# Kernel optimization log

Measured on AMD Instinct MI355X. Metric: run time of the kernel, lower is better.

Reference implementation:

```python
import jax, jax.numpy as jnp
import numpy as np
from jax import lax

B, T, H, F, K, NB, MAXLEN = 32, 1024, 384, 384, 3, 256, 2048


def _ln(x, g, b, eps=1e-5):
    m = jnp.mean(x, axis=-1, keepdims=True)
    v = jnp.var(x, axis=-1, keepdims=True)
    return (x - m) * lax.rsqrt(v + eps) * g + b


def _conv(x, w, b):
    # x: (B, T, Cin), w: (K, Cin, Cout); SAME padding == torch padding=(K-1)//2 for K=3, stride 1
    y = lax.conv_general_dilated(x, w, (1,), 'SAME', dimension_numbers=('NWC', 'WIO', 'NWC'))
    return y + b


def _predictor(x, mask, w1, b1, g1, be1, w2, b2, g2, be2, wo, bo):
    h = _ln(jax.nn.relu(_conv(x, w1, b1)), g1, be1)
    h = _ln(jax.nn.relu(_conv(h, w2, b2)), g2, be2)
    out = jnp.einsum('btf,f->bt', h, wo) + bo  # Linear(F -> 1).squeeze(-1)
    return jnp.where(mask, 0.0, out)


def _length_regulate(x, dur, max_len):
    # vectorized equivalent of torch per-sample expand+cat+pad
    csum = jnp.cumsum(dur, axis=1)                      # (B, T)
    total = csum[:, -1]                                 # (B,) = mel_len
    frames = jnp.arange(max_len)                        # (M,)
    # frame f belongs to phoneme i with csum[i-1] <= f < csum[i]
    idx = jax.vmap(lambda c: jnp.searchsorted(c, frames, side='right'))(csum)  # (B, M)
    idx = jnp.clip(idx, 0, x.shape[1] - 1)
    out = jnp.take_along_axis(x, idx[:, :, None], axis=1)                      # (B, M, H)
    valid = (frames[None, :] < total[:, None]).astype(x.dtype)                 # zero-pad tail
    return out * valid[:, :, None], total


def setup_inputs() -> dict:
    key = jax.random.key(0)
    ks = iter(jax.random.split(key, 64))
    nk = lambda: next(ks)
    d = {}
    d['x'] = jax.random.normal(nk(), (B, T, H), jnp.float32)
    d['src_mask'] = jnp.zeros((B, T), jnp.bool_)
    d['duration'] = jax.random.randint(nk(), (B, T), 0, 4)
    d['max_len'] = MAXLEN
    for p in ('dp', 'pp', 'ep'):
        d[p + '_w1'] = jax.random.normal(nk(), (K, H, F), jnp.float32) * 0.02
        d[p + '_b1'] = jnp.zeros((F,), jnp.float32)
        d[p + '_g1'] = jnp.ones((F,), jnp.float32)
        d[p + '_be1'] = jnp.zeros((F,), jnp.float32)
        d[p + '_w2'] = jax.random.normal(nk(), (K, F, F), jnp.float32) * 0.02
        d[p + '_b2'] = jnp.zeros((F,), jnp.float32)
        d[p + '_g2'] = jnp.ones((F,), jnp.float32)
        d[p + '_be2'] = jnp.zeros((F,), jnp.float32)
        d[p + '_wo'] = jax.random.normal(nk(), (F,), jnp.float32) * 0.02
        d[p + '_bo'] = jnp.zeros((1,), jnp.float32)
    d['pitch_bins'] = jnp.linspace(0.0, 1.0, NB - 1, dtype=jnp.float32)
    d['energy_bins'] = jnp.linspace(0.0, 1.0, NB - 1, dtype=jnp.float32)
    d['pitch_emb'] = jax.random.normal(nk(), (NB, H), jnp.float32) * 0.02
    d['energy_emb'] = jax.random.normal(nk(), (NB, H), jnp.float32) * 0.02
    d['pitch_target'] = jax.random.uniform(nk(), (B, T), jnp.float32)
    d['energy_target'] = jax.random.uniform(nk(), (B, T), jnp.float32)
    return d


def reference(x, src_mask, duration, max_len,
              dp_w1, dp_b1, dp_g1, dp_be1, dp_w2, dp_b2, dp_g2, dp_be2, dp_wo, dp_bo,
              pp_w1, pp_b1, pp_g1, pp_be1, pp_w2, pp_b2, pp_g2, pp_be2, pp_wo, pp_bo,
              ep_w1, ep_b1, ep_g1, ep_be1, ep_w2, ep_b2, ep_g2, ep_be2, ep_wo, ep_bo,
              pitch_bins, energy_bins, pitch_emb, energy_emb, pitch_target, energy_target):
    log_dur = _predictor(x, src_mask, dp_w1, dp_b1, dp_g1, dp_be1, dp_w2, dp_b2, dp_g2, dp_be2, dp_wo, dp_bo)
    # phoneme-level pitch (target path: bucketize target, torch.bucketize right=False == searchsorted left)
    pitch_pred = _predictor(x, src_mask, pp_w1, pp_b1, pp_g1, pp_be1, pp_w2, pp_b2, pp_g2, pp_be2, pp_wo, pp_bo)
    x = x + pitch_emb[jnp.searchsorted(pitch_bins, pitch_target, side='left')]
    # phoneme-level energy (predictor sees x AFTER pitch embedding add, as in torch)
    energy_pred = _predictor(x, src_mask, ep_w1, ep_b1, ep_g1, ep_be1, ep_w2, ep_b2, ep_g2, ep_be2, ep_wo, ep_bo)
    x = x + energy_emb[jnp.searchsorted(energy_bins, energy_target, side='left')]
    x_out, mel_len = _length_regulate(x, duration, max_len)
    return (x_out, pitch_pred, energy_pred, log_dur, mel_len)
```

## Files before the change

kernel.cpp:

```cpp
#include <hip/hip_runtime.h>

#define B_ 32
#define T_ 1024
#define C_ 384
#define MAXLEN_ 2048
#define NBINS_ 255
#define WPK1 442368
#define BTC  (32 * 1024 * 384)
#define ARS 392

typedef __attribute__((ext_vector_type(8))) short short8v;
typedef __attribute__((ext_vector_type(4))) float floatx4;

__device__ __forceinline__ unsigned short f2bf(float f) {
    unsigned u = __float_as_uint(f);
    u += 0x7fffu + ((u >> 16) & 1u);
    return (unsigned short)(u >> 16);
}

struct CvP {
    const float* xf;
    const unsigned short* xb;
    const unsigned short* wpk;
    const float* bias[3];
    const float* gamma[3];
    const float* beta[3];
    const float* wo[3];
    const float* bo[3];
    unsigned short* hout;
    float* pred[3];
    const float* pbins;
    const float* pemb;
    const float* ptgt;
    int final_flag;
};

__global__ __launch_bounds__(256, 2) void conv_mfma3(CvP P)
{
    __shared__ unsigned short As[66 * ARS];
    float* rsum = (float*)As;
    float* rsq  = rsum + 256;

    const int tid  = threadIdx.x;
    const int wave = tid >> 6;
    const int lane = tid & 63;
    const int lq   = lane >> 4;
    const int ln   = lane & 15;
    const int p    = blockIdx.x >> 9;
    const int bi   = blockIdx.x & 511;
    const int b    = bi >> 4;
    const int t0   = (bi & 15) << 6;
    const int nb   = wave * 96;

    const unsigned short* bbase =
        P.wpk + (size_t)p * WPK1 + wave * 3072 + (size_t)lane * 8;
    short8v bA[6], bB[6];
#pragma unroll
    for (int nt = 0; nt < 6; ++nt) {
        bA[nt] = *(const short8v*)(bbase + (nt << 9));
        bB[nt] = *(const short8v*)(bbase + 12288 + (nt << 9));
    }

    if (!P.final_flag) {
        const bool fuse_emb = (p == 2);
        for (int i = tid; i < 66 * 48; i += 256) {
            const int row = i / 48;
            const int c   = i - row * 48;
            const int t   = t0 - 1 + row;
            short8v v = (short8v){0,0,0,0,0,0,0,0};
            if ((unsigned)t < (unsigned)T_) {
                const float* sp = P.xf + ((size_t)(b << 10) + t) * C_ + c * 8;
                float f[8];
                *(float4*)&f[0] = *(const float4*)sp;
                *(float4*)&f[4] = *(const float4*)(sp + 4);
                if (fuse_emb) {
                    const float tg = P.ptgt[(b << 10) + t];
                    int lo = 0, hi = NBINS_;
                    while (lo < hi) {
                        const int mid = (lo + hi) >> 1;
                        if (P.pbins[mid] < tg) lo = mid + 1; else hi = mid;
                    }
                    const float* er = P.pemb + (size_t)lo * C_ + c * 8;
#pragma unroll
                    for (int j = 0; j < 8; ++j) f[j] += er[j];
                }
#pragma unroll
                for (int j = 0; j < 8; ++j) v[j] = (short)f2bf(f[j]);
            }
            *(short8v*)&As[row * ARS + c * 8] = v;
        }
    } else {
        const unsigned short* xb = P.xb + (size_t)p * BTC;
        for (int i = tid; i < 66 * 48; i += 256) {
            const int row = i / 48;
            const int c   = i - row * 48;
            const int t   = t0 - 1 + row;
            short8v v = (short8v){0,0,0,0,0,0,0,0};
            if ((unsigned)t < (unsigned)T_)
                v = *(const short8v*)(xb + ((size_t)(b << 10) + t) * C_ + c * 8);
            *(short8v*)&As[row * ARS + c * 8] = v;
        }
    }
    __syncthreads();

    floatx4 acc[24];
#pragma unroll
    for (int i = 0; i < 24; ++i) acc[i] = (floatx4){0.f, 0.f, 0.f, 0.f};

    const unsigned short* abase = &As[ln * ARS + lq * 8];
    const unsigned short* bpA = bbase + 2 * 12288;
    const unsigned short* bpB = bbase + 3 * 12288;

#pragma unroll
    for (int kc = 0; kc < 3; ++kc) {
#pragma unroll
        for (int h2 = 0; h2 < 6; ++h2) {
            const int hb = h2 * 64;
            const int r  = kc * 12 + h2 * 2;
            {
                short8v afrag[4];
#pragma unroll
                for (int mt = 0; mt < 4; ++mt)
                    afrag[mt] = *(const short8v*)(abase + (mt * 16 + kc) * ARS + hb);
#pragma unroll
                for (int mt = 0; mt < 4; ++mt)
#pragma unroll
                    for (int nt = 0; nt < 6; ++nt)
                        acc[mt * 6 + nt] = __builtin_amdgcn_mfma_f32_16x16x32_bf16(
                            afrag[mt], bA[nt], acc[mt * 6 + nt], 0, 0, 0);
                if (r + 2 < 36) {
#pragma unroll
                    for (int nt = 0; nt < 6; ++nt)
                        bA[nt] = *(const short8v*)(bpA + (nt << 9));
                    bpA += 24576;
                }
            }
            {
                short8v afrag[4];
#pragma unroll
                for (int mt = 0; mt < 4; ++mt)
                    afrag[mt] = *(const short8v*)(abase + (mt * 16 + kc) * ARS + hb + 32);
#pragma unroll
                for (int mt = 0; mt < 4; ++mt)
#pragma unroll
                    for (int nt = 0; nt < 6; ++nt)
                        acc[mt * 6 + nt] = __builtin_amdgcn_mfma_f32_16x16x32_bf16(
                            afrag[mt], bB[nt], acc[mt * 6 + nt], 0, 0, 0);
                if (r + 3 < 36) {
#pragma unroll
                    for (int nt = 0; nt < 6; ++nt)
                        bB[nt] = *(const short8v*)(bpB + (nt << 9));
                    bpB += 24576;
                }
            }
        }
    }
    __syncthreads();

    float bcol[6], gcol[6], becol[6], wcol[6];
#pragma unroll
    for (int nt = 0; nt < 6; ++nt) {
        const int col = nb + nt * 16 + ln;
        bcol[nt]  = P.bias[p][col];
        gcol[nt]  = P.gamma[p][col];
        becol[nt] = P.beta[p][col];
        wcol[nt]  = P.final_flag ? P.wo[p][col] : 0.f;
    }

#pragma unroll
    for (int mt = 0; mt < 4; ++mt) {
#pragma unroll
        for (int rg = 0; rg < 4; ++rg) {
            float s = 0.f, q = 0.f;
#pragma unroll
            for (int nt = 0; nt < 6; ++nt) {
                float v = acc[mt * 6 + nt][rg] + bcol[nt];
                v = v > 0.f ? v : 0.f;
                acc[mt * 6 + nt][rg] = v;
                s += v; q += v * v;
            }
#pragma unroll
            for (int off = 1; off < 16; off <<= 1) {
                s += __shfl_xor(s, off, 64);
                q += __shfl_xor(q, off, 64);
            }
            if (ln == mt * 4 + rg) {
                rsum[wave * 64 + mt * 16 + lq * 4 + rg] = s;
                rsq [wave * 64 + mt * 16 + lq * 4 + rg] = q;
            }
        }
    }
    __syncthreads();

    float mean_[16], rstd_[16];
#pragma unroll
    for (int mt = 0; mt < 4; ++mt) {
#pragma unroll
        for (int rg = 0; rg < 4; ++rg) {
            const int row = mt * 16 + lq * 4 + rg;
            const float s = rsum[row] + rsum[64 + row] + rsum[128 + row] + rsum[192 + row];
            const float q = rsq[row] + rsq[64 + row] + rsq[128 + row] + rsq[192 + row];
            const float m = s * (1.f / 384.f);
            const float var = q * (1.f / 384.f) - m * m;
            mean_[mt * 4 + rg] = m;
            rstd_[mt * 4 + rg] = rsqrtf(var + 1e-5f);
        }
    }

    if (!P.final_flag) {
        unsigned short* hout = P.hout + (size_t)p * BTC;
#pragma unroll
        for (int mt = 0; mt < 4; ++mt)
#pragma unroll
            for (int rg = 0; rg < 4; ++rg) {
                const float m = mean_[mt * 4 + rg], rs = rstd_[mt * 4 + rg];
                const int grow = (bi << 6) + mt * 16 + lq * 4 + rg;
#pragma unroll
                for (int nt = 0; nt < 6; ++nt) {
                    const float v = (acc[mt * 6 + nt][rg] - m) * rs * gcol[nt] + becol[nt];
                    hout[(size_t)grow * C_ + nb + nt * 16 + ln] = f2bf(v);
                }
            }
    } else {
        __syncthreads();
#pragma unroll
        for (int mt = 0; mt < 4; ++mt) {
#pragma unroll
            for (int rg = 0; rg < 4; ++rg) {
                const float m = mean_[mt * 4 + rg], rs = rstd_[mt * 4 + rg];
                float pr = 0.f;
#pragma unroll
                for (int nt = 0; nt < 6; ++nt)
                    pr += ((acc[mt * 6 + nt][rg] - m) * rs * gcol[nt] + becol[nt]) * wcol[nt];
#pragma unroll
                for (int off = 1; off < 16; off <<= 1)
                    pr += __shfl_xor(pr, off, 64);
                if (ln == mt * 4 + rg)
                    rsum[wave * 64 + mt * 16 + lq * 4 + rg] = pr;
            }
        }
        __syncthreads();
        if (tid < 64)
            P.pred[p][(bi << 6) + tid] =
                rsum[tid] + rsum[64 + tid] + rsum[128 + tid] + rsum[192 + tid] + P.bo[p][0];
    }
}

#define WSS 388
__global__ __launch_bounds__(256) void pack_w_kernel(
    const float* __restrict__ s0, const float* __restrict__ s1,
    const float* __restrict__ s2, const float* __restrict__ s3,
    const float* __restrict__ s4, const float* __restrict__ s5,
    unsigned short* __restrict__ dst)
{
    __shared__ float ws[32 * WSS];
    const int blk  = blockIdx.x;
    const int wsel = blk / 36;
    const int r    = blk - wsel * 36;
    const float* src = wsel == 0 ? s0 : wsel == 1 ? s1 : wsel == 2 ? s2
                     : wsel == 3 ? s3 : wsel == 4 ? s4 : s5;
    const int tid = threadIdx.x;

    const float* sb = src + (size_t)r * 32 * C_;
    for (int i4 = tid; i4 < 3072; i4 += 256) {
        const int k  = i4 / 96;
        const int n4 = i4 - k * 96;
        *(float4*)&ws[k * WSS + n4 * 4] = *(const float4*)(sb + (size_t)k * C_ + n4 * 4);
    }
    __syncthreads();

    unsigned short* db = dst + (size_t)wsel * WPK1 + (size_t)r * 12288;
    for (int c = tid; c < 1536; c += 256) {
        const int lane = c & 63;
        const int wnt  = c >> 6;
        const int ln   = lane & 15;
        const int lq   = lane >> 4;
        const int n    = (wnt / 6) * 96 + (wnt % 6) * 16 + ln;
        ushort4 o0, o1;
        unsigned short e[8];
#pragma unroll
        for (int j = 0; j < 8; ++j)
            e[j] = f2bf(ws[(lq * 8 + j) * WSS + n]);
        o0 = make_ushort4(e[0], e[1], e[2], e[3]);
        o1 = make_ushort4(e[4], e[5], e[6], e[7]);
        *(ushort4*)(db + wnt * 512 + lane * 8)     = o0;
        *(ushort4*)(db + wnt * 512 + lane * 8 + 4) = o1;
    }
}

__global__ __launch_bounds__(256) void cumsum_idx_kernel(
    const int* __restrict__ dur,
    const float* __restrict__ pbins, const float* __restrict__ ptgt,
    const float* __restrict__ ebins, const float* __restrict__ etgt,
    int* __restrict__ xidx, float* __restrict__ mel_len)
{
    __shared__ int cs[T_];
    __shared__ int part[256];
    __shared__ float pb[NBINS_], eb[NBINS_];
    const int b = blockIdx.x;
    const int tid = threadIdx.x;
    if (tid < NBINS_) { pb[tid] = pbins[tid]; eb[tid] = ebins[tid]; }
    int l[4];
    int s = 0;
#pragma unroll
    for (int i = 0; i < 4; ++i) { l[i] = dur[(b << 10) + tid * 4 + i]; s += l[i]; }
    part[tid] = s;
    __syncthreads();
    for (int off = 1; off < 256; off <<= 1) {
        int u = 0;
        if (tid >= off) u = part[tid - off];
        __syncthreads();
        part[tid] += u;
        __syncthreads();
    }
    const int incl = part[tid];
    int run = incl - s;
#pragma unroll
    for (int i = 0; i < 4; ++i) {
        run += l[i];
        cs[tid * 4 + i] = run;
    }
    if (tid == 255) mel_len[b] = (float)incl;
    __syncthreads();
    const int total = cs[T_ - 1];
    for (int f = tid; f < MAXLEN_; f += 256) {
        int pk = -1;
        if (f < total) {
            int lo = 0, hi = T_;
            while (lo < hi) {
                const int mid = (lo + hi) >> 1;
                if (cs[mid] <= f) lo = mid + 1; else hi = mid;
            }
            const int t = lo > T_ - 1 ? T_ - 1 : lo;
            const int row = (b << 10) + t;
            const float ptg = ptgt[row];
            int plo = 0, phi = NBINS_;
            while (plo < phi) {
                const int mid = (plo + phi) >> 1;
                if (pb[mid] < ptg) plo = mid + 1; else phi = mid;
            }
            const float etg = etgt[row];
            int elo = 0, ehi = NBINS_;
            while (elo < ehi) {
                const int mid = (elo + ehi) >> 1;
                if (eb[mid] < etg) elo = mid + 1; else ehi = mid;
            }
            pk = t | (plo << 10) | (elo << 19);
        }
        xidx[(b << 11) + f] = pk;
    }
}

__global__ __launch_bounds__(256) void length_reg_kernel(
    const float* __restrict__ x, const int* __restrict__ xidx,
    const float* __restrict__ pemb, const float* __restrict__ eemb,
    float* __restrict__ out)
{
    const int g    = blockIdx.x * 256 + threadIdx.x;
    const int c4   = g % 96;
    const int rest = g / 96;
    const int frame = rest & (MAXLEN_ - 1);
    const int b     = rest >> 11;
    const int pk = xidx[(b << 11) + frame];
    float4 v = make_float4(0.f, 0.f, 0.f, 0.f);
    if (pk >= 0) {
        const int t   = pk & 1023;
        const int plo = (pk >> 10) & 511;
        const int elo = (pk >> 19) & 511;
        v = *(const float4*)(x + ((size_t)(b << 10) + t) * C_ + c4 * 4);
        const float4 pe = *(const float4*)(pemb + (size_t)plo * C_ + c4 * 4);
        const float4 ee = *(const float4*)(eemb + (size_t)elo * C_ + c4 * 4);
        v.x += pe.x + ee.x; v.y += pe.y + ee.y;
        v.z += pe.z + ee.z; v.w += pe.w + ee.w;
    }
    *(float4*)(out + (size_t)g * 4) = v;
}

extern "C" void kernel_launch(void* const* d_in, const int* in_sizes, int n_in,
                              void* d_out, int out_size, void* d_ws, size_t ws_size,
                              hipStream_t stream)
{
    const float* x        = (const float*)d_in[0];
    const int*   duration = (const int*)d_in[2];
    const float* P[3][10];
    for (int p = 0; p < 3; ++p)
        for (int q = 0; q < 10; ++q)
            P[p][q] = (const float*)d_in[4 + p * 10 + q];
    const float* pitch_bins    = (const float*)d_in[34];
    const float* energy_bins   = (const float*)d_in[35];
    const float* pitch_emb     = (const float*)d_in[36];
    const float* energy_emb    = (const float*)d_in[37];
    const float* pitch_target  = (const float*)d_in[38];
    const float* energy_target = (const float*)d_in[39];

    float* out_x      = (float*)d_out;
    float* out_pitch  = out_x + (size_t)B_ * MAXLEN_ * C_;
    float* out_energy = out_pitch + B_ * T_;
    float* out_logdur = out_energy + B_ * T_;
    float* out_mellen = out_logdur + B_ * T_;

    unsigned short* h1b = (unsigned short*)out_x;

    unsigned short* wpk = (unsigned short*)d_ws;
    int* xidx = (int*)(wpk + (size_t)6 * WPK1);

    const dim3 blk(256);

    pack_w_kernel<<<216, blk, 0, stream>>>(
        P[0][0], P[0][4], P[1][0], P[1][4], P[2][0], P[2][4], wpk);

    CvP P1;
    P1.xf = x; P1.xb = nullptr; P1.wpk = wpk;
    for (int p = 0; p < 3; ++p) {
        P1.bias[p]  = P[p][1];
        P1.gamma[p] = P[p][2];
        P1.beta[p]  = P[p][3];
        P1.wo[p]    = nullptr;
        P1.bo[p]    = nullptr;
        P1.pred[p]  = nullptr;
    }
    P1.hout = h1b;
    P1.pbins = pitch_bins; P1.pemb = pitch_emb; P1.ptgt = pitch_target;
    P1.final_flag = 0;

    CvP P2;
    P2.xf = nullptr; P2.xb = h1b; P2.wpk = wpk + (size_t)3 * WPK1;
    for (int p = 0; p < 3; ++p) {
        P2.bias[p]  = P[p][5];
        P2.gamma[p] = P[p][6];
        P2.beta[p]  = P[p][7];
        P2.wo[p]    = P[p][8];
        P2.bo[p]    = P[p][9];
    }
    P2.pred[0] = out_logdur; P2.pred[1] = out_pitch; P2.pred[2] = out_energy;
    P2.hout = nullptr;
    P2.pbins = nullptr; P2.pemb = nullptr; P2.ptgt = nullptr;
    P2.final_flag = 1;

    conv_mfma3<<<1536, blk, 0, stream>>>(P1);
    conv_mfma3<<<1536, blk, 0, stream>>>(P2);

    cumsum_idx_kernel<<<B_, blk, 0, stream>>>(
        duration, pitch_bins, pitch_target, energy_bins, energy_target,
        xidx, out_mellen);
    length_reg_kernel<<<24576, blk, 0, stream>>>(
        x, xidx, pitch_emb, energy_emb, out_x);
}
```

Before: 467.6 us.

## Split conv N-dimension across six waves and hoist pitch bucketize per row

```diff
diff --git a/kernel.cpp b/kernel.cpp
--- a/kernel.cpp
+++ b/kernel.cpp
@@ -35,11 +35,12 @@
     int final_flag;
 };
 
-__global__ __launch_bounds__(256, 2) void conv_mfma3(CvP P)
+__global__ __launch_bounds__(384, 3) void conv_mfma3(CvP P)
 {
     __shared__ unsigned short As[66 * ARS];
+    __shared__ int embi[66];
     float* rsum = (float*)As;
-    float* rsq  = rsum + 256;
+    float* rsq  = rsum + 384;
 
     const int tid  = threadIdx.x;
     const int wave = tid >> 6;
@@ -50,48 +51,60 @@
     const int bi   = blockIdx.x & 511;
     const int b    = bi >> 4;
     const int t0   = (bi & 15) << 6;
-    const int nb   = wave * 96;
+    const int nb   = wave << 6;
 
     const unsigned short* bbase =
-        P.wpk + (size_t)p * WPK1 + wave * 3072 + (size_t)lane * 8;
-    short8v bA[6], bB[6];
-#pragma unroll
-    for (int nt = 0; nt < 6; ++nt) {
+        P.wpk + (size_t)p * WPK1 + (size_t)(wave << 11) + (size_t)lane * 8;
+    short8v bA[4], bB[4];
+#pragma unroll
+    for (int nt = 0; nt < 4; ++nt) {
         bA[nt] = *(const short8v*)(bbase + (nt << 9));
         bB[nt] = *(const short8v*)(bbase + 12288 + (nt << 9));
     }
 
     if (!P.final_flag) {
         const bool fuse_emb = (p == 2);
-        for (int i = tid; i < 66 * 48; i += 256) {
+        if (fuse_emb) {
+            if (tid < 66) {
+                const int t = t0 - 1 + tid;
+                int lo = 0;
+                if ((unsigned)t < (unsigned)T_) {
+                    const float tg = P.ptgt[(b << 10) + t];
+                    int hi = NBINS_;
+                    while (lo < hi) {
+                        const int mid = (lo + hi) >> 1;
+                        if (P.pbins[mid] < tg) lo = mid + 1; else hi = mid;
+                    }
+                }
+                embi[tid] = lo;
+            }
+            __syncthreads();
+        }
+        for (int i = tid; i < 66 * 48; i += 384) {
             const int row = i / 48;
             const int c   = i - row * 48;
             const int t   = t0 - 1 + row;
-            short8v v = (short8v){0,0,0,0,0,0,0,0};
+            uint4 pv = make_uint4(0u, 0u, 0u, 0u);
             if ((unsigned)t < (unsigned)T_) {
                 const float* sp = P.xf + ((size_t)(b << 10) + t) * C_ + c * 8;
                 float f[8];
                 *(float4*)&f[0] = *(const float4*)sp;
                 *(float4*)&f[4] = *(const float4*)(sp + 4);
                 if (fuse_emb) {
-                    const float tg = P.ptgt[(b << 10) + t];
-                    int lo = 0, hi = NBINS_;
-                    while (lo < hi) {
-                        const int mid = (lo + hi) >> 1;
-                        if (P.pbins[mid] < tg) lo = mid + 1; else hi = mid;
-                    }
-                    const float* er = P.pemb + (size_t)lo * C_ + c * 8;
+                    const float* er = P.pemb + (size_t)embi[row] * C_ + c * 8;
 #pragma unroll
                     for (int j = 0; j < 8; ++j) f[j] += er[j];
                 }
-#pragma unroll
-                for (int j = 0; j < 8; ++j) v[j] = (short)f2bf(f[j]);
-            }
-            *(short8v*)&As[row * ARS + c * 8] = v;
+                asm("v_cvt_pk_bf16_f32 %0, %1, %2" : "=v"(pv.x) : "v"(f[0]), "v"(f[1]));
+                asm("v_cvt_pk_bf16_f32 %0, %1, %2" : "=v"(pv.y) : "v"(f[2]), "v"(f[3]));
+                asm("v_cvt_pk_bf16_f32 %0, %1, %2" : "=v"(pv.z) : "v"(f[4]), "v"(f[5]));
+                asm("v_cvt_pk_bf16_f32 %0, %1, %2" : "=v"(pv.w) : "v"(f[6]), "v"(f[7]));
+            }
+            *(uint4*)&As[row * ARS + c * 8] = pv;
         }
     } else {
         const unsigned short* xb = P.xb + (size_t)p * BTC;
-        for (int i = tid; i < 66 * 48; i += 256) {
+        for (int i = tid; i < 66 * 48; i += 384) {
             const int row = i / 48;
             const int c   = i - row * 48;
             const int t   = t0 - 1 + row;
@@ -103,9 +116,9 @@
     }
     __syncthreads();
 
-    floatx4 acc[24];
-#pragma unroll
-    for (int i = 0; i < 24; ++i) acc[i] = (floatx4){0.f, 0.f, 0.f, 0.f};
+    floatx4 acc[16];
+#pragma unroll
+    for (int i = 0; i < 16; ++i) acc[i] = (floatx4){0.f, 0.f, 0.f, 0.f};
 
     const unsigned short* abase = &As[ln * ARS + lq * 8];
     const unsigned short* bpA = bbase + 2 * 12288;
@@ -125,12 +138,12 @@
 #pragma unroll
                 for (int mt = 0; mt < 4; ++mt)
 #pragma unroll
-                    for (int nt = 0; nt < 6; ++nt)
-                        acc[mt * 6 + nt] = __builtin_amdgcn_mfma_f32_16x16x32_bf16(
-                            afrag[mt], bA[nt], acc[mt * 6 + nt], 0, 0, 0);
+                    for (int nt = 0; nt < 4; ++nt)
+                        acc[mt * 4 + nt] = __builtin_amdgcn_mfma_f32_16x16x32_bf16(
+                            afrag[mt], bA[nt], acc[mt * 4 + nt], 0, 0, 0);
                 if (r + 2 < 36) {
 #pragma unroll
-                    for (int nt = 0; nt < 6; ++nt)
+                    for (int nt = 0; nt < 4; ++nt)
                         bA[nt] = *(const short8v*)(bpA + (nt << 9));
                     bpA += 24576;
                 }
@@ -143,12 +156,12 @@
 #pragma unroll
                 for (int mt = 0; mt < 4; ++mt)
 #pragma unroll
-                    for (int nt = 0; nt < 6; ++nt)
-                        acc[mt * 6 + nt] = __builtin_amdgcn_mfma_f32_16x16x32_bf16(
-                            afrag[mt], bB[nt], acc[mt * 6 + nt], 0, 0, 0);
+                    for (int nt = 0; nt < 4; ++nt)
+                        acc[mt * 4 + nt] = __builtin_amdgcn_mfma_f32_16x16x32_bf16(
+                            afrag[mt], bB[nt], acc[mt * 4 + nt], 0, 0, 0);
                 if (r + 3 < 36) {
 #pragma unroll
-                    for (int nt = 0; nt < 6; ++nt)
+                    for (int nt = 0; nt < 4; ++nt)
                         bB[nt] = *(const short8v*)(bpB + (nt << 9));
                     bpB += 24576;
                 }
@@ -157,9 +170,9 @@
     }
     __syncthreads();
 
-    float bcol[6], gcol[6], becol[6], wcol[6];
-#pragma unroll
-    for (int nt = 0; nt < 6; ++nt) {
+    float bcol[4], gcol[4], becol[4], wcol[4];
+#pragma unroll
+    for (int nt = 0; nt < 4; ++nt) {
         const int col = nb + nt * 16 + ln;
         bcol[nt]  = P.bias[p][col];
         gcol[nt]  = P.gamma[p][col];
@@ -173,10 +186,10 @@
         for (int rg = 0; rg < 4; ++rg) {
             float s = 0.f, q = 0.f;
 #pragma unroll
-            for (int nt = 0; nt < 6; ++nt) {
-                float v = acc[mt * 6 + nt][rg] + bcol[nt];
+            for (int nt = 0; nt < 4; ++nt) {
+                float v = acc[mt * 4 + nt][rg] + bcol[nt];
                 v = v > 0.f ? v : 0.f;
-                acc[mt * 6 + nt][rg] = v;
+                acc[mt * 4 + nt][rg] = v;
                 s += v; q += v * v;
             }
 #pragma unroll
@@ -198,8 +211,12 @@
 #pragma unroll
         for (int rg = 0; rg < 4; ++rg) {
             const int row = mt * 16 + lq * 4 + rg;
-            const float s = rsum[row] + rsum[64 + row] + rsum[128 + row] + rsum[192 + row];
-            const float q = rsq[row] + rsq[64 + row] + rsq[128 + row] + rsq[192 + row];
+            float s = 0.f, q = 0.f;
+#pragma unroll
+            for (int w = 0; w < 6; ++w) {
+                s += rsum[w * 64 + row];
+                q += rsq [w * 64 + row];
+            }
             const float m = s * (1.f / 384.f);
             const float var = q * (1.f / 384.f) - m * m;
             mean_[mt * 4 + rg] = m;
@@ -215,10 +232,15 @@
             for (int rg = 0; rg < 4; ++rg) {
                 const float m = mean_[mt * 4 + rg], rs = rstd_[mt * 4 + rg];
                 const int grow = (bi << 6) + mt * 16 + lq * 4 + rg;
-#pragma unroll
-                for (int nt = 0; nt < 6; ++nt) {
-                    const float v = (acc[mt * 6 + nt][rg] - m) * rs * gcol[nt] + becol[nt];
-                    hout[(size_t)grow * C_ + nb + nt * 16 + ln] = f2bf(v);
+                unsigned short* hb_ = hout + (size_t)grow * C_ + nb + ln;
+#pragma unroll
+                for (int n2 = 0; n2 < 2; ++n2) {
+                    const float v0 = (acc[mt * 4 + n2 * 2    ][rg] - m) * rs * gcol[n2 * 2    ] + becol[n2 * 2    ];
+                    const float v1 = (acc[mt * 4 + n2 * 2 + 1][rg] - m) * rs * gcol[n2 * 2 + 1] + becol[n2 * 2 + 1];
+                    unsigned u;
+                    asm("v_cvt_pk_bf16_f32 %0, %1, %2" : "=v"(u) : "v"(v0), "v"(v1));
+                    hb_[(n2 * 2) * 16]     = (unsigned short)(u & 0xffffu);
+                    hb_[(n2 * 2 + 1) * 16] = (unsigned short)(u >> 16);
                 }
             }
     } else {
@@ -230,8 +252,8 @@
                 const float m = mean_[mt * 4 + rg], rs = rstd_[mt * 4 + rg];
                 float pr = 0.f;
 #pragma unroll
-                for (int nt = 0; nt < 6; ++nt)
-                    pr += ((acc[mt * 6 + nt][rg] - m) * rs * gcol[nt] + becol[nt]) * wcol[nt];
+                for (int nt = 0; nt < 4; ++nt)
+                    pr += ((acc[mt * 4 + nt][rg] - m) * rs * gcol[nt] + becol[nt]) * wcol[nt];
 #pragma unroll
                 for (int off = 1; off < 16; off <<= 1)
                     pr += __shfl_xor(pr, off, 64);
@@ -240,9 +262,12 @@
             }
         }
         __syncthreads();
-        if (tid < 64)
-            P.pred[p][(bi << 6) + tid] =
-                rsum[tid] + rsum[64 + tid] + rsum[128 + tid] + rsum[192 + tid] + P.bo[p][0];
+        if (tid < 64) {
+            float s = P.bo[p][0];
+#pragma unroll
+            for (int w = 0; w < 6; ++w) s += rsum[w * 64 + tid];
+            P.pred[p][(bi << 6) + tid] = s;
+        }
     }
 }
 
@@ -275,7 +300,7 @@
         const int wnt  = c >> 6;
         const int ln   = lane & 15;
         const int lq   = lane >> 4;
-        const int n    = (wnt / 6) * 96 + (wnt % 6) * 16 + ln;
+        const int n    = wnt * 16 + ln;
         ushort4 o0, o1;
         unsigned short e[8];
 #pragma unroll
@@ -405,6 +430,7 @@
     int* xidx = (int*)(wpk + (size_t)6 * WPK1);
 
     const dim3 blk(256);
+    const dim3 cblk(384);
 
     pack_w_kernel<<<216, blk, 0, stream>>>(
         P[0][0], P[0][4], P[1][0], P[1][4], P[2][0], P[2][4], wpk);
@@ -437,8 +463,8 @@
     P2.pbins = nullptr; P2.pemb = nullptr; P2.ptgt = nullptr;
     P2.final_flag = 1;
 
-    conv_mfma3<<<1536, blk, 0, stream>>>(P1);
-    conv_mfma3<<<1536, blk, 0, stream>>>(P2);
+    conv_mfma3<<<1536, cblk, 0, stream>>>(P1);
+    conv_mfma3<<<1536, cblk, 0, stream>>>(P2);
 
     cumsum_idx_kernel<<<B_, blk, 0, stream>>>(
         duration, pitch_bins, pitch_target, energy_bins, energy_target,
```

New measurement: 543.1 us. 16.2% more time.
